# Performance work log

Hardware: AMD Instinct MI355X
Metric: run time of the kernel (lower is better)

Reference implementation:

```python
import jax, jax.numpy as jnp
import numpy as np

B, N = 2, 256
IN_N = 32          # input node features
H = 8              # per-layer default num_heads (GAT does not override it)
HN, HE = 64, 64    # hidden node / edge features per head
DN, DE = HN * H, HE * H  # 512, 512
OUT_N = 32


def _gat_layer(nodes, edges, mask, Wn, bn, We, be, Wa):
    # nodes: [b,n,dn_in], edges: [b,n,n,de_in], mask: [b,n] bool
    nf = nodes @ Wn + bn                                   # [b,n,DN]
    ef = jnp.einsum('bije,ef->bijf', edges, We) + be       # [b,n,n,DE]
    q = nf @ Wa                                            # [b,n,H]
    qe = jnp.einsum('bijf,fh->bijh', ef, Wa)               # [b,n,n,H]
    sn = jnp.einsum('bik,bjk->bij', q, q) / np.float32(np.sqrt(HN))
    se = jnp.einsum('bik,bijk->bij', q, qe) / np.float32(np.sqrt(HE))
    m = mask[..., None]
    wn = jax.nn.softmax(sn * m, axis=-1)                   # [b,n,n]
    we = jax.nn.softmax(se * m, axis=-1)                   # [b,n,n]
    awn = jnp.einsum('bij,bik->bjk', wn, nf)               # [b,n,DN]
    agg_e = jnp.einsum('bij,bijk->bik', we, ef)            # [b,n,DE]
    upd_nodes = nf + awn + agg_e                           # [b,n,DN]
    upd_edges = ef + we[..., None] * ef + jnp.einsum('bij,bik->bijk', wn, nf)
    re = jax.nn.elu(upd_edges)                             # [b,n,n,DE]
    re = (re + jnp.swapaxes(re, 1, 2)) / 2
    return jax.nn.elu(upd_nodes), re


def setup_inputs() -> dict:
    key = jax.random.key(0)
    ks = jax.random.split(key, 16)
    s = 0.05
    return {
        'nodes': jax.random.normal(ks[0], (B, N, IN_N), jnp.float32),
        'edges': jax.random.normal(ks[1], (B, N, N), jnp.float32),
        'node_mask': jnp.ones((B, N), dtype=bool),
        # layer 1 params
        'Wn1': jax.random.normal(ks[2], (IN_N, DN), jnp.float32) * s,
        'bn1': jnp.zeros((DN,), jnp.float32),
        'We1': jax.random.normal(ks[3], (1, DE), jnp.float32) * s,
        'be1': jnp.zeros((DE,), jnp.float32),
        'Wa1': jax.random.normal(ks[4], (DN, H), jnp.float32) * s,
        # layer 2 params
        'Wn2': jax.random.normal(ks[5], (DN, DN), jnp.float32) * s,
        'bn2': jnp.zeros((DN,), jnp.float32),
        'We2': jax.random.normal(ks[6], (DE, DE), jnp.float32) * s,
        'be2': jnp.zeros((DE,), jnp.float32),
        'Wa2': jax.random.normal(ks[7], (DN, H), jnp.float32) * s,
        # final projections
        'Wfn': jax.random.normal(ks[8], (DN, OUT_N), jnp.float32) * s,
        'bfn': jnp.zeros((OUT_N,), jnp.float32),
        'Wfe': jax.random.normal(ks[9], (DE, 1), jnp.float32) * s,
        'bfe': jnp.zeros((1,), jnp.float32),
    }


def reference(nodes, edges, node_mask, Wn1, bn1, We1, be1, Wa1,
              Wn2, bn2, We2, be2, Wa2, Wfn, bfn, Wfe, bfe):
    e = edges[..., None]                      # [b,n,n,1]
    e = (e + jnp.swapaxes(e, 1, 2)) / 2       # symmetrize
    e = jax.nn.relu(e)
    n, e = _gat_layer(nodes, e, node_mask, Wn1, bn1, We1, be1, Wa1)
    n, e = _gat_layer(n, e, node_mask, Wn2, bn2, We2, be2, Wa2)
    out_nodes = jnp.tanh(n @ Wfn + bfn)                                   # [b,n,OUT_N]
    out_edges = jnp.tanh(jnp.einsum('bijf,fo->bijo', e, Wfe) + bfe)[..., 0]  # [b,n,n]
    return out_nodes, out_edges
```

## Files before the change

kernel.cpp:

```cpp
#include <hip/hip_runtime.h>
#include <hip/hip_bf16.h>
#include <stdint.h>


typedef __attribute__((ext_vector_type(8))) short short8v;
typedef __attribute__((ext_vector_type(4))) float f32x4;

#define AS1 __attribute__((address_space(1)))
#define AS3 __attribute__((address_space(3)))

__device__ __forceinline__ float eluf(float x) { return x > 0.f ? x : (__expf(x) - 1.f); }

__device__ __forceinline__ short f2bf(float x) {
  union { float f; unsigned u; } v; v.f = x;
  unsigned r = v.u + 0x7fffu + ((v.u >> 16) & 1u);
  return (short)(r >> 16);
}

template<int OP>
__device__ float blockRed256(float v, float* s4) {
#pragma unroll
  for (int o = 32; o; o >>= 1) { float t = __shfl_xor(v, o); v = OP ? fmaxf(v, t) : v + t; }
  int w = threadIdx.x >> 6;
  __syncthreads();
  if ((threadIdx.x & 63) == 0) s4[w] = v;
  __syncthreads();
  return OP ? fmaxf(fmaxf(s4[0], s4[1]), fmaxf(s4[2], s4[3]))
            : (s4[0] + s4[1] + s4[2] + s4[3]);
}

__global__ void k0a_pack(const float* __restrict__ We2, short* __restrict__ Bp) {
  int id = blockIdx.x * 256 + threadIdx.x;
  int c = id >> 11; int rem = id & 2047; int g = rem >> 9; int n = rem & 511;
  short8v v;
#pragma unroll
  for (int e = 0; e < 8; e++) v[e] = f2bf(We2[(c * 32 + g * 8 + e) * 512 + n]);
  int pos = n * 4 + (g ^ ((n >> 1) & 3));
  *(short8v*)(Bp + (c * 2048 + pos) * 8) = v;
}

__global__ void k0b_prep(const float* __restrict__ We2, const float* __restrict__ Wa2,
                         const float* __restrict__ We1, const float* __restrict__ be1,
                         const float* __restrict__ be2, const float* __restrict__ Wa1,
                         float* __restrict__ M2, float* __restrict__ u1,
                         float* __restrict__ v1, float* __restrict__ vb2) {
  int bx = blockIdx.x; int lane = threadIdx.x;
  if (bx < 512) {
    float a[8] = {0, 0, 0, 0, 0, 0, 0, 0};
    for (int k0 = lane; k0 < 512; k0 += 64) {
      float wv = We2[bx * 512 + k0];
      const float* wa = Wa2 + k0 * 8;
#pragma unroll
      for (int h = 0; h < 8; h++) a[h] += wv * wa[h];
    }
#pragma unroll
    for (int h = 0; h < 8; h++) {
      float v = a[h];
      for (int o = 32; o; o >>= 1) v += __shfl_xor(v, o);
      if (lane == 0) M2[bx * 8 + h] = v;
    }
  } else {
    const float* src = (bx == 512) ? We1 : (bx == 513 ? be1 : be2);
    const float* Wa = (bx == 514) ? Wa2 : Wa1;
    float* dst = (bx == 512) ? u1 : (bx == 513 ? v1 : vb2);
    float a[8] = {0, 0, 0, 0, 0, 0, 0, 0};
    for (int f = lane; f < 512; f += 64) {
      float s = src[f];
#pragma unroll
      for (int h = 0; h < 8; h++) a[h] += s * Wa[f * 8 + h];
    }
#pragma unroll
    for (int h = 0; h < 8; h++) {
      float v = a[h];
      for (int o = 32; o; o >>= 1) v += __shfl_xor(v, o);
      if (lane == 0) dst[h] = v;
    }
  }
}

__global__ __launch_bounds__(512) void k1_nf1(const float* __restrict__ nodes,
    const float* __restrict__ Wn1, const float* __restrict__ bn1,
    const float* __restrict__ Wa1, float* __restrict__ nf1, float* __restrict__ q1) {
  __shared__ float nrow[32];
  __shared__ float qL[8];
  int bi = blockIdx.x; int f = threadIdx.x;
  if (f < 32) nrow[f] = nodes[bi * 32 + f];
  if (f < 8) qL[f] = 0.f;
  __syncthreads();
  float acc = bn1[f];
#pragma unroll 8
  for (int c = 0; c < 32; c++) acc += nrow[c] * Wn1[c * 512 + f];
  nf1[bi * 512 + f] = acc;
  const float* wa = Wa1 + f * 8;
#pragma unroll
  for (int h = 0; h < 8; h++) {
    float v = acc * wa[h];
    for (int o = 32; o; o >>= 1) v += __shfl_xor(v, o);
    if ((f & 63) == 0) atomicAdd(&qL[h], v);
  }
  __syncthreads();
  if (f < 8) q1[bi * 8 + f] = qL[f];
}

__global__ __launch_bounds__(256) void k2_l1attn(const float* __restrict__ edges,
    const float* __restrict__ q1, const float* __restrict__ u1, const float* __restrict__ v1,
    float* __restrict__ e0, float* __restrict__ wn1, float* __restrict__ we1,
    float* __restrict__ tt) {
  __shared__ float s4[4];
  int bi = blockIdx.x; int b = bi >> 8; int i = bi & 255; int j = threadIdx.x;
  float qi[8], qj[8];
#pragma unroll
  for (int h = 0; h < 8; h++) { qi[h] = q1[bi * 8 + h]; qj[h] = q1[(b * 256 + j) * 8 + h]; }
  float eij = edges[bi * 256 + j];
  float eji = edges[(b * 256 + j) * 256 + i];
  float e0v = fmaxf(0.f, 0.5f * (eij + eji));
  e0[bi * 256 + j] = e0v;
  float sn = 0.f, aI = 0.f, cI = 0.f;
#pragma unroll
  for (int h = 0; h < 8; h++) { sn += qi[h] * qj[h]; aI += qi[h] * u1[h]; cI += qi[h] * v1[h]; }
  sn *= 0.125f;
  float se = (aI * e0v + cI) * 0.125f;
  float mn = blockRed256<1>(sn, s4);
  float en = __expf(sn - mn);
  float sumn = blockRed256<0>(en, s4);
  float wnv = en / sumn; wn1[bi * 256 + j] = wnv;
  float me = blockRed256<1>(se, s4);
  float ee = __expf(se - me);
  float sume = blockRed256<0>(ee, s4);
  float wev = ee / sume; we1[bi * 256 + j] = wev;
  float t = blockRed256<0>(wev * e0v, s4);
  if (j == 0) tt[bi] = t;
}

__global__ __launch_bounds__(512) void k3_n1(const float* __restrict__ nf1,
    const float* __restrict__ wn1, const float* __restrict__ tt,
    const float* __restrict__ We1, const float* __restrict__ be1, float* __restrict__ n1) {
  int bx = blockIdx.x; int b = bx >> 8; int x = bx & 255; int k = threadIdx.x;
  float acc = 0.f;
#pragma unroll 4
  for (int i = 0; i < 256; i++) {
    float w = wn1[(b * 256 + i) * 256 + x];
    acc += w * nf1[(b * 256 + i) * 512 + k];
  }
  float t = tt[bx];
  float v = nf1[bx * 512 + k] + acc + t * We1[k] + be1[k];
  n1[bx * 512 + k] = eluf(v);
}

__global__ __launch_bounds__(512) void k4_nf2(const float* __restrict__ n1,
    const float* __restrict__ Wn2, const float* __restrict__ bn2,
    const float* __restrict__ Wa2, const float* __restrict__ M2, const float* __restrict__ vb2,
    float* __restrict__ nf2, float* __restrict__ q2, float* __restrict__ p2,
    float* __restrict__ cst) {
  __shared__ float rowL[512];
  __shared__ float qL[8];
  int bi = blockIdx.x; int k = threadIdx.x;
  rowL[k] = n1[bi * 512 + k];
  if (k < 8) qL[k] = 0.f;
  __syncthreads();
  float acc = bn2[k];
#pragma unroll 4
  for (int g = 0; g < 512; g++) acc += rowL[g] * Wn2[g * 512 + k];
  nf2[bi * 512 + k] = acc;
  const float* wa = Wa2 + k * 8;
#pragma unroll
  for (int h = 0; h < 8; h++) {
    float v = acc * wa[h];
    for (int o = 32; o; o >>= 1) v += __shfl_xor(v, o);
    if ((k & 63) == 0) atomicAdd(&qL[h], v);
  }
  __syncthreads();
  float q[8];
#pragma unroll
  for (int h = 0; h < 8; h++) q[h] = qL[h];
  if (k < 8) q2[bi * 8 + k] = q[k];
  float pv = 0.f; const float* m2 = M2 + k * 8;
#pragma unroll
  for (int h = 0; h < 8; h++) pv += m2[h] * q[h];
  p2[bi * 512 + k] = pv;
  if (k == 0) {
    float c = 0.f;
#pragma unroll
    for (int h = 0; h < 8; h++) c += q[h] * vb2[h];
    cst[bi] = c;
  }
}

__global__ __launch_bounds__(256) void k5a_wn2(const float* __restrict__ q2,
                                               float* __restrict__ wn2) {
  __shared__ float s4[4];
  int bi = blockIdx.x; int b = bi >> 8; int j = threadIdx.x;
  float sn = 0.f;
#pragma unroll
  for (int h = 0; h < 8; h++) sn += q2[bi * 8 + h] * q2[(b * 256 + j) * 8 + h];
  sn *= 0.125f;
  float mn = blockRed256<1>(sn, s4);
  float en = __expf(sn - mn);
  float s = blockRed256<0>(en, s4);
  wn2[bi * 256 + j] = en / s;
}

__global__ __launch_bounds__(256) void k5b_we2(const float* __restrict__ nf1,
    const float* __restrict__ p2, const float* __restrict__ e0,
    const float* __restrict__ wn1, const float* __restrict__ we1,
    const float* __restrict__ We1, const float* __restrict__ be1,
    const float* __restrict__ cst, float* __restrict__ we2) {
  __shared__ float nfiL[512], p2L[512], We1L[512], be1L[512], seL[256], s4[4];
  int bi = blockIdx.x; int b = bi >> 8; int i = bi & 255;
  int tid = threadIdx.x, lane = tid & 63, w = tid >> 6;
  for (int t = tid; t < 512; t += 256) {
    nfiL[t] = nf1[bi * 512 + t]; p2L[t] = p2[bi * 512 + t];
    We1L[t] = We1[t]; be1L[t] = be1[t];
  }
  __syncthreads();
  float cstv = cst[bi];
  int f0 = lane * 8;
  for (int jj = 0; jj < 64; jj++) {
    int j = w * 64 + jj;
    int ij = bi * 256 + j, ji = (b * 256 + j) * 256 + i;
    float e0v = e0[ij];
    float s1 = 1.f + we1[ij]; float w1 = wn1[ij];
    float s2 = 1.f + we1[ji]; float w2 = wn1[ji];
    const float* nj = nf1 + (b * 256 + j) * 512 + f0;
    float4 b0 = *(const float4*)nj;
    float4 b1 = *(const float4*)(nj + 4);
    float njv[8] = {b0.x, b0.y, b0.z, b0.w, b1.x, b1.y, b1.z, b1.w};
    float dot = 0.f;
#pragma unroll
    for (int e = 0; e < 8; e++) {
      float ef = e0v * We1L[f0 + e] + be1L[f0 + e];
      float x1 = ef * s1 + w1 * nfiL[f0 + e];
      float x2 = ef * s2 + w2 * njv[e];
      float e1v = 0.5f * (eluf(x1) + eluf(x2));
      dot += e1v * p2L[f0 + e];
    }
#pragma unroll
    for (int o = 32; o; o >>= 1) dot += __shfl_xor(dot, o);
    if (lane == 0) seL[j] = (dot + cstv) * 0.125f;
  }
  __syncthreads();
  float se = seL[tid];
  float m = blockRed256<1>(se, s4);
  float ee = __expf(se - m);
  float s = blockRed256<0>(ee, s4);
  we2[bi * 256 + tid] = ee / s;
}

__global__ __launch_bounds__(512, 2) void k6_main(
    const float* __restrict__ nf1, const float* __restrict__ nf2,
    const float* __restrict__ e0, const float* __restrict__ wn1, const float* __restrict__ we1,
    const float* __restrict__ wn2, const float* __restrict__ we2,
    const float* __restrict__ We1, const float* __restrict__ be1, const float* __restrict__ be2,
    const float* __restrict__ Wfe, const short* __restrict__ Bp,
    float* __restrict__ aggp, float* __restrict__ Dout) {
  __shared__ __align__(16) short As[4096];
  __shared__ __align__(16) short Bs[16384];
  __shared__ float nf1iL[512], We1L[512], be1L[512], nf2L[512], be2L[512], WfeL[512];
  __shared__ float e0r[128], s1r[128], wnir[128], s2r[128], wnjr[128], weR[128], wnR[128];
  float* aggL = (float*)As;
  float* dsumL = aggL + 512;

  int bid = blockIdx.x; int jb = bid & 1; int bi = bid >> 1; int b = bi >> 8; int i = bi & 255;
  int tid = threadIdx.x, lane = tid & 63, w = tid >> 6;
  int wm = w >> 2, wn_ = w & 3;
  int jbase = jb * 128;

  {
    int t = tid;
    nf1iL[t] = nf1[bi * 512 + t]; We1L[t] = We1[t]; be1L[t] = be1[t];
    nf2L[t] = nf2[bi * 512 + t]; be2L[t] = be2[t]; WfeL[t] = Wfe[t];
  }
  if (tid < 128) {
    int j = jbase + tid; int ij = bi * 256 + j; int ji = (b * 256 + j) * 256 + i;
    e0r[tid] = e0[ij]; s1r[tid] = 1.f + we1[ij]; wnir[tid] = wn1[ij];
    s2r[tid] = 1.f + we1[ji]; wnjr[tid] = wn1[ji];
    weR[tid] = we2[ij]; wnR[tid] = wn2[ij];
  }
  __syncthreads();

  f32x4 acc[4][8];
#pragma unroll
  for (int mi = 0; mi < 4; mi++)
#pragma unroll
    for (int nf = 0; nf < 8; nf++) acc[mi][nf] = (f32x4){0.f, 0.f, 0.f, 0.f};

  int ar = tid >> 2;
  int ac = tid & 3;
  const float* njbase = nf1 + (size_t)(b * 256 + jbase + ar) * 512;
  float e0v = e0r[ar], s1 = s1r[ar], w1 = wnir[ar], s2 = s2r[ar], w2 = wnjr[ar];
  int apos = ar * 4 + (ac ^ ((ar >> 1) & 3));

  for (int cg = 0; cg < 16; cg++) {
    if (cg) __syncthreads();
    {
      const char* g = (const char*)(Bp + cg * 16384);
      char* l = (char*)Bs;
#pragma unroll
      for (int it = 0; it < 4; ++it) {
        int off = it * 8192 + w * 1024;
        __builtin_amdgcn_global_load_lds(
            (const AS1 void*)(g + off + lane * 16),
            (AS3 void*)(l + off), 16, 0, 0);
      }
    }
    {
      int f0 = cg * 32 + ac * 8;
      const float* nj = njbase + f0;
      float4 g0 = *(const float4*)nj;
      float4 g1 = *(const float4*)(nj + 4);
      float njv[8] = {g0.x, g0.y, g0.z, g0.w, g1.x, g1.y, g1.z, g1.w};
      float Wv[8], bv[8], niv[8];
      *(float4*)&Wv[0] = *(const float4*)&We1L[f0]; *(float4*)&Wv[4] = *(const float4*)&We1L[f0 + 4];
      *(float4*)&bv[0] = *(const float4*)&be1L[f0]; *(float4*)&bv[4] = *(const float4*)&be1L[f0 + 4];
      *(float4*)&niv[0] = *(const float4*)&nf1iL[f0]; *(float4*)&niv[4] = *(const float4*)&nf1iL[f0 + 4];
      short8v pk;
#pragma unroll
      for (int e = 0; e < 8; e++) {
        float ef = e0v * Wv[e] + bv[e];
        float x1 = ef * s1 + w1 * niv[e];
        float x2 = ef * s2 + w2 * njv[e];
        float v = 0.5f * (eluf(x1) + eluf(x2));
        pk[e] = f2bf(v);
      }
      *(short8v*)(As + apos * 8) = pk;
    }
    __syncthreads();

    short8v a[4];
    int g_ = lane >> 4;
#pragma unroll
    for (int mi = 0; mi < 4; mi++) {
      int row = wm * 64 + mi * 16 + (lane & 15);
      int cpos = row * 4 + (g_ ^ ((row >> 1) & 3));
      a[mi] = *(const short8v*)(As + cpos * 8);
    }
#pragma unroll
    for (int nf = 0; nf < 8; nf++) {
      int n = wn_ * 128 + nf * 16 + (lane & 15);
      int pos = n * 4 + (g_ ^ ((n >> 1) & 3));
      short8v bf = *(const short8v*)(Bs + pos * 8);
#pragma unroll
      for (int mi = 0; mi < 4; mi++)
        acc[mi][nf] = __builtin_amdgcn_mfma_f32_16x16x32_bf16(a[mi], bf, acc[mi][nf], 0, 0, 0);
    }
  }

  __syncthreads();
  aggL[tid] = 0.f;
  if (tid < 128) dsumL[tid] = 0.f;
  __syncthreads();

  float be2v[8], wfev[8], nf2v[8];
#pragma unroll
  for (int nf = 0; nf < 8; nf++) {
    int k = wn_ * 128 + nf * 16 + (lane & 15);
    be2v[nf] = be2L[k]; wfev[nf] = WfeL[k]; nf2v[nf] = nf2L[k];
  }
  float aggv[8] = {0, 0, 0, 0, 0, 0, 0, 0};
#pragma unroll
  for (int mi = 0; mi < 4; mi++) {
#pragma unroll
    for (int r = 0; r < 4; r++) {
      int jl = wm * 64 + mi * 16 + (lane >> 4) * 4 + r;
      float wE = weR[jl], wN = wnR[jl]; float sE = 1.f + wE;
      float dv = 0.f;
#pragma unroll
      for (int nf = 0; nf < 8; nf++) {
        float ef2 = acc[mi][nf][r] + be2v[nf];
        aggv[nf] += wE * ef2;
        float U = ef2 * sE + wN * nf2v[nf];
        dv += eluf(U) * wfev[nf];
      }
#pragma unroll
      for (int o = 1; o < 16; o <<= 1) dv += __shfl_xor(dv, o);
      if ((lane & 15) == 0) atomicAdd(&dsumL[jl], dv);
    }
  }
#pragma unroll
  for (int nf = 0; nf < 8; nf++) {
    float v = aggv[nf];
    v += __shfl_xor(v, 16); v += __shfl_xor(v, 32);
    if (lane < 16) atomicAdd(&aggL[wn_ * 128 + nf * 16 + lane], v);
  }
  __syncthreads();
  aggp[(bi * 2 + jb) * 512 + tid] = aggL[tid];
  if (tid < 128) Dout[bi * 256 + jbase + tid] = dsumL[tid];
}

__global__ __launch_bounds__(512) void k7_n2(const float* __restrict__ nf2,
    const float* __restrict__ wn2, const float* __restrict__ aggp, float* __restrict__ n2) {
  int bx = blockIdx.x; int b = bx >> 8; int x = bx & 255; int k = threadIdx.x;
  float acc = 0.f;
#pragma unroll 4
  for (int i = 0; i < 256; i++) {
    float w = wn2[(b * 256 + i) * 256 + x];
    acc += w * nf2[(b * 256 + i) * 512 + k];
  }
  float agg = aggp[(bx * 2 + 0) * 512 + k] + aggp[(bx * 2 + 1) * 512 + k];
  n2[bx * 512 + k] = eluf(nf2[bx * 512 + k] + acc + agg);
}

__global__ __launch_bounds__(256) void k8_outn(const float* __restrict__ n2,
    const float* __restrict__ Wfn, const float* __restrict__ bfn, float* __restrict__ outn) {
  __shared__ float rowL[512];
  __shared__ float red[256];
  int bi = blockIdx.x; int tid = threadIdx.x;
  rowL[tid] = n2[bi * 512 + tid];
  rowL[tid + 256] = n2[bi * 512 + tid + 256];
  __syncthreads();
  int o = tid & 31, part = tid >> 5;
  float acc = 0.f;
  for (int f = part * 64; f < part * 64 + 64; f++) acc += rowL[f] * Wfn[f * 32 + o];
  red[tid] = acc;
  __syncthreads();
  if (tid < 32) {
    float s = 0.f;
#pragma unroll
    for (int p = 0; p < 8; p++) s += red[p * 32 + tid];
    outn[bi * 32 + tid] = tanhf(s + bfn[tid]);
  }
}

__global__ __launch_bounds__(256) void k9_oute(const float* __restrict__ D,
    const float* __restrict__ bfe, float* __restrict__ oute) {
  int bi = blockIdx.x; int b = bi >> 8; int i = bi & 255; int j = threadIdx.x;
  float v = 0.5f * (D[bi * 256 + j] + D[(b * 256 + j) * 256 + i]) + bfe[0];
  oute[bi * 256 + j] = tanhf(v);
}

extern "C" void kernel_launch(void* const* d_in, const int* in_sizes, int n_in,
                              void* d_out, int out_size, void* d_ws, size_t ws_size,
                              hipStream_t stream) {
  const float* nodes = (const float*)d_in[0];
  const float* edges = (const float*)d_in[1];
  const float* Wn1 = (const float*)d_in[3];
  const float* bn1 = (const float*)d_in[4];
  const float* We1 = (const float*)d_in[5];
  const float* be1 = (const float*)d_in[6];
  const float* Wa1 = (const float*)d_in[7];
  const float* Wn2 = (const float*)d_in[8];
  const float* bn2 = (const float*)d_in[9];
  const float* We2 = (const float*)d_in[10];
  const float* be2 = (const float*)d_in[11];
  const float* Wa2 = (const float*)d_in[12];
  const float* Wfn = (const float*)d_in[13];
  const float* bfn = (const float*)d_in[14];
  const float* Wfe = (const float*)d_in[15];
  const float* bfe = (const float*)d_in[16];

  float* ws = (float*)d_ws;
  size_t off = 0;
  float* nf1 = ws + off; off += 262144;
  float* q1 = ws + off; off += 4096;
  float* e0 = ws + off; off += 131072;
  float* wn1 = ws + off; off += 131072;
  float* we1 = ws + off; off += 131072;
  float* tt = ws + off; off += 512;
  float* n1 = ws + off; off += 262144;
  float* nf2 = ws + off; off += 262144;
  float* q2 = ws + off; off += 4096;
  float* p2 = ws + off; off += 262144;
  float* cst = ws + off; off += 512;
  float* wn2 = ws + off; off += 131072;
  float* we2 = ws + off; off += 131072;
  float* M2 = ws + off; off += 4096;
  float* u1 = ws + off; off += 8;
  float* v1 = ws + off; off += 8;
  float* vb2 = ws + off; off += 16;
  float* aggp = ws + off; off += 524288;
  float* Dm = ws + off; off += 131072;
  float* n2 = ws + off; off += 262144;
  short* Bp = (short*)(ws + off); off += 131072;

  float* outn = (float*)d_out;
  float* oute = outn + 2 * 256 * 32;

  hipLaunchKernelGGL(k0a_pack, dim3(128), dim3(256), 0, stream, We2, Bp);
  hipLaunchKernelGGL(k0b_prep, dim3(515), dim3(64), 0, stream, We2, Wa2, We1, be1, be2, Wa1,
                     M2, u1, v1, vb2);
  hipLaunchKernelGGL(k1_nf1, dim3(512), dim3(512), 0, stream, nodes, Wn1, bn1, Wa1, nf1, q1);
  hipLaunchKernelGGL(k2_l1attn, dim3(512), dim3(256), 0, stream, edges, q1, u1, v1, e0, wn1,
                     we1, tt);
  hipLaunchKernelGGL(k3_n1, dim3(512), dim3(512), 0, stream, nf1, wn1, tt, We1, be1, n1);
  hipLaunchKernelGGL(k4_nf2, dim3(512), dim3(512), 0, stream, n1, Wn2, bn2, Wa2, M2, vb2,
                     nf2, q2, p2, cst);
  hipLaunchKernelGGL(k5a_wn2, dim3(512), dim3(256), 0, stream, q2, wn2);
  hipLaunchKernelGGL(k5b_we2, dim3(512), dim3(256), 0, stream, nf1, p2, e0, wn1, we1, We1,
                     be1, cst, we2);
  hipLaunchKernelGGL(k6_main, dim3(1024), dim3(512), 0, stream, nf1, nf2, e0, wn1, we1, wn2,
                     we2, We1, be1, be2, Wfe, Bp, aggp, Dm);
  hipLaunchKernelGGL(k7_n2, dim3(512), dim3(512), 0, stream, nf2, wn2, aggp, n2);
  hipLaunchKernelGGL(k8_outn, dim3(512), dim3(256), 0, stream, n2, Wfn, bfn, outn);
  hipLaunchKernelGGL(k9_oute, dim3(512), dim3(256), 0, stream, Dm, bfe, oute);
}
```

Baseline: 306.8 us.

## Exploit edge symmetry: compute each (i,j)/(j,i) tile pair once in k5b and k6

The layer-2 edge-score and main edge GEMM kernels now iterate over upper-triangular 16x16 tile pairs. The symmetric layer-1 edge feature is built once and reused for both the (i,j) and (j,i) outputs, which roughly halves the GEMM and elementwise work. Node aggregation now goes through global atomics into a zero-initialised buffer. The k3, k4 and k7 node kernels each process two rows per block so weight loads are shared, and k6 occupancy hints are raised. The costs are atomic contention, a memset, a serial triangular index decode, and register pressure from the dual epilogue.

```diff
diff --git a/kernel.cpp b/kernel.cpp
--- a/kernel.cpp
+++ b/kernel.cpp
@@ -135,16 +135,20 @@
 __global__ __launch_bounds__(512) void k3_n1(const float* __restrict__ nf1,
     const float* __restrict__ wn1, const float* __restrict__ tt,
     const float* __restrict__ We1, const float* __restrict__ be1, float* __restrict__ n1) {
-  int bx = blockIdx.x; int b = bx >> 8; int x = bx & 255; int k = threadIdx.x;
-  float acc = 0.f;
+  int bx = blockIdx.x;
+  int b = bx >> 7; int x0 = (bx & 127) * 2; int k = threadIdx.x;
+  float acc0 = 0.f, acc1 = 0.f;
 #pragma unroll 4
   for (int i = 0; i < 256; i++) {
-    float w = wn1[(b * 256 + i) * 256 + x];
-    acc += w * nf1[(b * 256 + i) * 512 + k];
-  }
-  float t = tt[bx];
-  float v = nf1[bx * 512 + k] + acc + t * We1[k] + be1[k];
-  n1[bx * 512 + k] = eluf(v);
+    float nv = nf1[(b * 256 + i) * 512 + k];
+    acc0 += wn1[(b * 256 + i) * 256 + x0] * nv;
+    acc1 += wn1[(b * 256 + i) * 256 + x0 + 1] * nv;
+  }
+  float w = We1[k], be = be1[k];
+  int g0 = b * 256 + x0;
+  n1[(size_t)g0 * 512 + k] = eluf(nf1[(size_t)g0 * 512 + k] + acc0 + tt[g0] * w + be);
+  n1[(size_t)(g0 + 1) * 512 + k] =
+      eluf(nf1[(size_t)(g0 + 1) * 512 + k] + acc1 + tt[g0 + 1] * w + be);
 }
 
 __global__ __launch_bounds__(512) void k4_nf2(const float* __restrict__ n1,
@@ -152,42 +156,109 @@
     const float* __restrict__ Wa2, const float* __restrict__ M2, const float* __restrict__ vb2,
     float* __restrict__ nf2, float* __restrict__ q2, float* __restrict__ p2,
     float* __restrict__ cst) {
-  __shared__ float rowL[512];
-  __shared__ float qL[8];
-  int bi = blockIdx.x; int k = threadIdx.x;
-  rowL[k] = n1[bi * 512 + k];
-  if (k < 8) qL[k] = 0.f;
-  __syncthreads();
-  float acc = bn2[k];
+  __shared__ float qL[2][8];
+  int bx = blockIdx.x;
+  int r0 = bx * 2, r1 = r0 + 1;
+  int k = threadIdx.x;
+  if (k < 16) qL[k >> 3][k & 7] = 0.f;
+  __syncthreads();
+  const float* a = n1 + (size_t)r0 * 512;
+  const float* c = n1 + (size_t)r1 * 512;
+  float acc0 = bn2[k], acc1 = bn2[k];
 #pragma unroll 4
-  for (int g = 0; g < 512; g++) acc += rowL[g] * Wn2[g * 512 + k];
-  nf2[bi * 512 + k] = acc;
+  for (int g = 0; g < 512; g++) {
+    float w = Wn2[g * 512 + k];
+    acc0 += a[g] * w; acc1 += c[g] * w;
+  }
+  nf2[(size_t)r0 * 512 + k] = acc0;
+  nf2[(size_t)r1 * 512 + k] = acc1;
   const float* wa = Wa2 + k * 8;
 #pragma unroll
   for (int h = 0; h < 8; h++) {
-    float v = acc * wa[h];
-    for (int o = 32; o; o >>= 1) v += __shfl_xor(v, o);
-    if ((k & 63) == 0) atomicAdd(&qL[h], v);
-  }
-  __syncthreads();
-  float q[8];
-#pragma unroll
-  for (int h = 0; h < 8; h++) q[h] = qL[h];
-  if (k < 8) q2[bi * 8 + k] = q[k];
-  float pv = 0.f; const float* m2 = M2 + k * 8;
-#pragma unroll
-  for (int h = 0; h < 8; h++) pv += m2[h] * q[h];
-  p2[bi * 512 + k] = pv;
+    float v0 = acc0 * wa[h], v1 = acc1 * wa[h];
+    for (int o = 32; o; o >>= 1) { v0 += __shfl_xor(v0, o); v1 += __shfl_xor(v1, o); }
+    if ((k & 63) == 0) { atomicAdd(&qL[0][h], v0); atomicAdd(&qL[1][h], v1); }
+  }
+  __syncthreads();
+  float q0[8], q1v[8];
+#pragma unroll
+  for (int h = 0; h < 8; h++) { q0[h] = qL[0][h]; q1v[h] = qL[1][h]; }
+  if (k < 8) { q2[r0 * 8 + k] = q0[k]; q2[r1 * 8 + k] = q1v[k]; }
+  float p0 = 0.f, p1 = 0.f; const float* m2 = M2 + k * 8;
+#pragma unroll
+  for (int h = 0; h < 8; h++) { p0 += m2[h] * q0[h]; p1 += m2[h] * q1v[h]; }
+  p2[(size_t)r0 * 512 + k] = p0;
+  p2[(size_t)r1 * 512 + k] = p1;
   if (k == 0) {
-    float c = 0.f;
-#pragma unroll
-    for (int h = 0; h < 8; h++) c += q[h] * vb2[h];
-    cst[bi] = c;
-  }
-}
-
-__global__ __launch_bounds__(256) void k5a_wn2(const float* __restrict__ q2,
-                                               float* __restrict__ wn2) {
+    float c0 = 0.f, c1 = 0.f;
+#pragma unroll
+    for (int h = 0; h < 8; h++) { c0 += q0[h] * vb2[h]; c1 += q1v[h] * vb2[h]; }
+    cst[r0] = c0; cst[r1] = c1;
+  }
+}
+
+__global__ __launch_bounds__(256) void k5b_pairs(const float* __restrict__ nf1,
+    const float* __restrict__ p2, const float* __restrict__ e0,
+    const float* __restrict__ wn1, const float* __restrict__ we1,
+    const float* __restrict__ We1, const float* __restrict__ be1,
+    const float* __restrict__ cst, float* __restrict__ se2) {
+  __shared__ float NI[16 * 132], NJ[16 * 132], PI[16 * 132], PJ[16 * 132];
+  __shared__ float W1[128], B1[128];
+  int bid = blockIdx.x; int b = bid & 1; int pr = bid >> 1;
+  int I = 0;
+  { int p = pr; while (p >= 16 - I) { p -= 16 - I; I++; } pr = p; }
+  int J = I + pr;
+  int I0 = I * 16, J0 = J * 16;
+  int tid = threadIdx.x; int ii = tid & 15, jj = tid >> 4;
+  int gi = b * 256 + I0 + ii, gj = b * 256 + J0 + jj;
+  int ij = gi * 256 + (J0 + jj), ji = gj * 256 + (I0 + ii);
+  float e0v = e0[ij];
+  float s1 = 1.f + we1[ij], w1 = wn1[ij];
+  float s2 = 1.f + we1[ji], w2 = wn1[ji];
+  float dot1 = 0.f, dot2 = 0.f;
+  for (int fc = 0; fc < 4; fc++) {
+    __syncthreads();
+    int f00 = fc * 128;
+    for (int t = tid; t < 2048; t += 256) {
+      int row = t >> 7, f = t & 127;
+      NI[row * 132 + f] = nf1[(size_t)(b * 256 + I0 + row) * 512 + f00 + f];
+      NJ[row * 132 + f] = nf1[(size_t)(b * 256 + J0 + row) * 512 + f00 + f];
+      PI[row * 132 + f] = p2[(size_t)(b * 256 + I0 + row) * 512 + f00 + f];
+      PJ[row * 132 + f] = p2[(size_t)(b * 256 + J0 + row) * 512 + f00 + f];
+    }
+    if (tid < 128) { W1[tid] = We1[f00 + tid]; B1[tid] = be1[f00 + tid]; }
+    __syncthreads();
+#pragma unroll 8
+    for (int f = 0; f < 128; f += 4) {
+      float4 niv = *(const float4*)&NI[ii * 132 + f];
+      float4 njv = *(const float4*)&NJ[jj * 132 + f];
+      float4 piv = *(const float4*)&PI[ii * 132 + f];
+      float4 pjv = *(const float4*)&PJ[jj * 132 + f];
+      float4 wv = *(const float4*)&W1[f];
+      float4 bv = *(const float4*)&B1[f];
+      float ni_[4] = {niv.x, niv.y, niv.z, niv.w};
+      float nj_[4] = {njv.x, njv.y, njv.z, njv.w};
+      float pi_[4] = {piv.x, piv.y, piv.z, piv.w};
+      float pj_[4] = {pjv.x, pjv.y, pjv.z, pjv.w};
+      float w_[4] = {wv.x, wv.y, wv.z, wv.w};
+      float b_[4] = {bv.x, bv.y, bv.z, bv.w};
+#pragma unroll
+      for (int e = 0; e < 4; e++) {
+        float ef = e0v * w_[e] + b_[e];
+        float x1 = ef * s1 + w1 * ni_[e];
+        float x2 = ef * s2 + w2 * nj_[e];
+        float e1v = 0.5f * (eluf(x1) + eluf(x2));
+        dot1 += e1v * pi_[e];
+        dot2 += e1v * pj_[e];
+      }
+    }
+  }
+  se2[ij] = (dot1 + cst[gi]) * 0.125f;
+  se2[ji] = (dot2 + cst[gj]) * 0.125f;
+}
+
+__global__ __launch_bounds__(256) void k5ac(const float* __restrict__ q2,
+    const float* __restrict__ se2, float* __restrict__ wn2, float* __restrict__ we2) {
   __shared__ float s4[4];
   int bi = blockIdx.x; int b = bi >> 8; int j = threadIdx.x;
   float sn = 0.f;
@@ -198,83 +269,51 @@
   float en = __expf(sn - mn);
   float s = blockRed256<0>(en, s4);
   wn2[bi * 256 + j] = en / s;
-}
-
-__global__ __launch_bounds__(256) void k5b_we2(const float* __restrict__ nf1,
-    const float* __restrict__ p2, const float* __restrict__ e0,
-    const float* __restrict__ wn1, const float* __restrict__ we1,
-    const float* __restrict__ We1, const float* __restrict__ be1,
-    const float* __restrict__ cst, float* __restrict__ we2) {
-  __shared__ float nfiL[512], p2L[512], We1L[512], be1L[512], seL[256], s4[4];
-  int bi = blockIdx.x; int b = bi >> 8; int i = bi & 255;
-  int tid = threadIdx.x, lane = tid & 63, w = tid >> 6;
-  for (int t = tid; t < 512; t += 256) {
-    nfiL[t] = nf1[bi * 512 + t]; p2L[t] = p2[bi * 512 + t];
-    We1L[t] = We1[t]; be1L[t] = be1[t];
-  }
-  __syncthreads();
-  float cstv = cst[bi];
-  int f0 = lane * 8;
-  for (int jj = 0; jj < 64; jj++) {
-    int j = w * 64 + jj;
-    int ij = bi * 256 + j, ji = (b * 256 + j) * 256 + i;
-    float e0v = e0[ij];
-    float s1 = 1.f + we1[ij]; float w1 = wn1[ij];
-    float s2 = 1.f + we1[ji]; float w2 = wn1[ji];
-    const float* nj = nf1 + (b * 256 + j) * 512 + f0;
-    float4 b0 = *(const float4*)nj;
-    float4 b1 = *(const float4*)(nj + 4);
-    float njv[8] = {b0.x, b0.y, b0.z, b0.w, b1.x, b1.y, b1.z, b1.w};
-    float dot = 0.f;
-#pragma unroll
-    for (int e = 0; e < 8; e++) {
-      float ef = e0v * We1L[f0 + e] + be1L[f0 + e];
-      float x1 = ef * s1 + w1 * nfiL[f0 + e];
-      float x2 = ef * s2 + w2 * njv[e];
-      float e1v = 0.5f * (eluf(x1) + eluf(x2));
-      dot += e1v * p2L[f0 + e];
-    }
-#pragma unroll
-    for (int o = 32; o; o >>= 1) dot += __shfl_xor(dot, o);
-    if (lane == 0) seL[j] = (dot + cstv) * 0.125f;
-  }
-  __syncthreads();
-  float se = seL[tid];
-  float m = blockRed256<1>(se, s4);
-  float ee = __expf(se - m);
-  float s = blockRed256<0>(ee, s4);
-  we2[bi * 256 + tid] = ee / s;
-}
-
-__global__ __launch_bounds__(512, 2) void k6_main(
+  float se = se2[bi * 256 + j];
+  float me = blockRed256<1>(se, s4);
+  float ee = __expf(se - me);
+  float s2 = blockRed256<0>(ee, s4);
+  we2[bi * 256 + j] = ee / s2;
+}
+
+__global__ __launch_bounds__(512, 4) void k6_main(
     const float* __restrict__ nf1, const float* __restrict__ nf2,
     const float* __restrict__ e0, const float* __restrict__ wn1, const float* __restrict__ we1,
     const float* __restrict__ wn2, const float* __restrict__ we2,
     const float* __restrict__ We1, const float* __restrict__ be1, const float* __restrict__ be2,
     const float* __restrict__ Wfe, const short* __restrict__ Bp,
-    float* __restrict__ aggp, float* __restrict__ Dout) {
-  __shared__ __align__(16) short As[4096];
-  __shared__ __align__(16) short Bs[16384];
-  __shared__ float nf1iL[512], We1L[512], be1L[512], nf2L[512], be2L[512], WfeL[512];
-  __shared__ float e0r[128], s1r[128], wnir[128], s2r[128], wnjr[128], weR[128], wnR[128];
-  float* aggL = (float*)As;
-  float* dsumL = aggL + 512;
-
-  int bid = blockIdx.x; int jb = bid & 1; int bi = bid >> 1; int b = bi >> 8; int i = bi & 255;
+    float* __restrict__ agg, float* __restrict__ Dout) {
+  __shared__ __align__(16) char region[40960];
+  short* As = (short*)region;
+  short* Bs = (short*)(region + 8192);
+  float* aggI_L = (float*)region;
+  __shared__ float We1L[512], be1L[512];
+  __shared__ float e0r[128], s1r[128], w1r[128], s2r[128], w2r[128];
+  __shared__ float weAr[128], wnAr[128], weBr[128], wnBr[128];
+  __shared__ float dsumA[128], dsumB[128];
+
+  int bid = blockIdx.x;
+  int b = bid & 1; int rest = bid >> 1;
+  int Jh = rest & 1; int pr = rest >> 1;
+  int I = 0;
+  { int p = pr; while (p >= 16 - I) { p -= 16 - I; I++; } pr = p; }
+  int J = I + pr;
+  int I0 = I * 16, J0 = J * 16 + Jh * 8;
+  bool dual = (I != J);
+
   int tid = threadIdx.x, lane = tid & 63, w = tid >> 6;
   int wm = w >> 2, wn_ = w & 3;
-  int jbase = jb * 128;
-
-  {
-    int t = tid;
-    nf1iL[t] = nf1[bi * 512 + t]; We1L[t] = We1[t]; be1L[t] = be1[t];
-    nf2L[t] = nf2[bi * 512 + t]; be2L[t] = be2[t]; WfeL[t] = Wfe[t];
-  }
+  int g4 = lane >> 4;
+
+  We1L[tid] = We1[tid]; be1L[tid] = be1[tid];
   if (tid < 128) {
-    int j = jbase + tid; int ij = bi * 256 + j; int ji = (b * 256 + j) * 256 + i;
-    e0r[tid] = e0[ij]; s1r[tid] = 1.f + we1[ij]; wnir[tid] = wn1[ij];
-    s2r[tid] = 1.f + we1[ji]; wnjr[tid] = wn1[ji];
-    weR[tid] = we2[ij]; wnR[tid] = wn2[ij];
+    int i = I0 + (tid & 15), j = J0 + (tid >> 4);
+    int ij = (b * 256 + i) * 256 + j, ji = (b * 256 + j) * 256 + i;
+    e0r[tid] = e0[ij];
+    s1r[tid] = 1.f + we1[ij]; w1r[tid] = wn1[ij];
+    s2r[tid] = 1.f + we1[ji]; w2r[tid] = wn1[ji];
+    weAr[tid] = we2[ij]; wnAr[tid] = wn2[ij];
+    weBr[tid] = we2[ji]; wnBr[tid] = wn2[ji];
   }
   __syncthreads();
 
@@ -286,8 +325,9 @@
 
   int ar = tid >> 2;
   int ac = tid & 3;
-  const float* njbase = nf1 + (size_t)(b * 256 + jbase + ar) * 512;
-  float e0v = e0r[ar], s1 = s1r[ar], w1 = wnir[ar], s2 = s2r[ar], w2 = wnjr[ar];
+  const float* nib = nf1 + (size_t)(b * 256 + I0 + (ar & 15)) * 512;
+  const float* njb = nf1 + (size_t)(b * 256 + J0 + (ar >> 4)) * 512;
+  float e0v = e0r[ar], s1 = s1r[ar], w1 = w1r[ar], s2 = s2r[ar], w2 = w2r[ar];
   int apos = ar * 4 + (ac ^ ((ar >> 1) & 3));
 
   for (int cg = 0; cg < 16; cg++) {
@@ -305,14 +345,17 @@
     }
     {
       int f0 = cg * 32 + ac * 8;
-      const float* nj = njbase + f0;
-      float4 g0 = *(const float4*)nj;
-      float4 g1 = *(const float4*)(nj + 4);
-      float njv[8] = {g0.x, g0.y, g0.z, g0.w, g1.x, g1.y, g1.z, g1.w};
-      float Wv[8], bv[8], niv[8];
-      *(float4*)&Wv[0] = *(const float4*)&We1L[f0]; *(float4*)&Wv[4] = *(const float4*)&We1L[f0 + 4];
-      *(float4*)&bv[0] = *(const float4*)&be1L[f0]; *(float4*)&bv[4] = *(const float4*)&be1L[f0 + 4];
-      *(float4*)&niv[0] = *(const float4*)&nf1iL[f0]; *(float4*)&niv[4] = *(const float4*)&nf1iL[f0 + 4];
+      float4 gi0 = *(const float4*)(nib + f0);
+      float4 gi1 = *(const float4*)(nib + f0 + 4);
+      float4 gj0 = *(const float4*)(njb + f0);
+      float4 gj1 = *(const float4*)(njb + f0 + 4);
+      float niv[8] = {gi0.x, gi0.y, gi0.z, gi0.w, gi1.x, gi1.y, gi1.z, gi1.w};
+      float njv[8] = {gj0.x, gj0.y, gj0.z, gj0.w, gj1.x, gj1.y, gj1.z, gj1.w};
+      float Wv[8], bv[8];
+      *(float4*)&Wv[0] = *(const float4*)&We1L[f0];
+      *(float4*)&Wv[4] = *(const float4*)&We1L[f0 + 4];
+      *(float4*)&bv[0] = *(const float4*)&be1L[f0];
+      *(float4*)&bv[4] = *(const float4*)&be1L[f0 + 4];
       short8v pk;
 #pragma unroll
       for (int e = 0; e < 8; e++) {
@@ -327,17 +370,16 @@
     __syncthreads();
 
     short8v a[4];
-    int g_ = lane >> 4;
 #pragma unroll
     for (int mi = 0; mi < 4; mi++) {
       int row = wm * 64 + mi * 16 + (lane & 15);
-      int cpos = row * 4 + (g_ ^ ((row >> 1) & 3));
+      int cpos = row * 4 + (g4 ^ ((row >> 1) & 3));
       a[mi] = *(const short8v*)(As + cpos * 8);
     }
 #pragma unroll
     for (int nf = 0; nf < 8; nf++) {
       int n = wn_ * 128 + nf * 16 + (lane & 15);
-      int pos = n * 4 + (g_ ^ ((n >> 1) & 3));
+      int pos = n * 4 + (g4 ^ ((n >> 1) & 3));
       short8v bf = *(const short8v*)(Bs + pos * 8);
 #pragma unroll
       for (int mi = 0; mi < 4; mi++)
@@ -346,58 +388,109 @@
   }
 
   __syncthreads();
-  aggL[tid] = 0.f;
-  if (tid < 128) dsumL[tid] = 0.f;
-  __syncthreads();
-
-  float be2v[8], wfev[8], nf2v[8];
+  if (tid < 128) { dsumA[tid] = 0.f; dsumB[tid] = 0.f; }
+  __syncthreads();
+
+  float be2v[8], wfev[8];
 #pragma unroll
   for (int nf = 0; nf < 8; nf++) {
     int k = wn_ * 128 + nf * 16 + (lane & 15);
-    be2v[nf] = be2L[k]; wfev[nf] = WfeL[k]; nf2v[nf] = nf2L[k];
-  }
-  float aggv[8] = {0, 0, 0, 0, 0, 0, 0, 0};
+    be2v[nf] = be2[k]; wfev[nf] = Wfe[k];
+  }
+  float aggI[4][8];
+#pragma unroll
+  for (int r4 = 0; r4 < 4; r4++)
+#pragma unroll
+    for (int nf = 0; nf < 8; nf++) aggI[r4][nf] = 0.f;
+
 #pragma unroll
   for (int mi = 0; mi < 4; mi++) {
-#pragma unroll
-    for (int r = 0; r < 4; r++) {
-      int jl = wm * 64 + mi * 16 + (lane >> 4) * 4 + r;
-      float wE = weR[jl], wN = wnR[jl]; float sE = 1.f + wE;
-      float dv = 0.f;
+    int jRow = J0 + wm * 4 + mi;
+    const float* nf2j = nf2 + (size_t)(b * 256 + jRow) * 512;
+    float aggJv[8] = {0, 0, 0, 0, 0, 0, 0, 0};
+#pragma unroll
+    for (int r4 = 0; r4 < 4; r4++) {
+      int jl = wm * 64 + mi * 16 + g4 * 4 + r4;
+      int iRow = I0 + g4 * 4 + r4;
+      const float* nf2i = nf2 + (size_t)(b * 256 + iRow) * 512;
+      float wEA = weAr[jl], sEA = 1.f + weAr[jl], wNA = wnAr[jl];
+      float wEB = weBr[jl], sEB = 1.f + weBr[jl], wNB = wnBr[jl];
+      float dvA = 0.f, dvB = 0.f;
 #pragma unroll
       for (int nf = 0; nf < 8; nf++) {
-        float ef2 = acc[mi][nf][r] + be2v[nf];
-        aggv[nf] += wE * ef2;
-        float U = ef2 * sE + wN * nf2v[nf];
-        dv += eluf(U) * wfev[nf];
+        int k = wn_ * 128 + nf * 16 + (lane & 15);
+        float ef2 = acc[mi][nf][r4] + be2v[nf];
+        aggI[r4][nf] += wEA * ef2;
+        float UA = ef2 * sEA + wNA * nf2i[k];
+        dvA += eluf(UA) * wfev[nf];
+        if (dual) {
+          aggJv[nf] += wEB * ef2;
+          float UB = ef2 * sEB + wNB * nf2j[k];
+          dvB += eluf(UB) * wfev[nf];
+        }
       }
 #pragma unroll
-      for (int o = 1; o < 16; o <<= 1) dv += __shfl_xor(dv, o);
-      if ((lane & 15) == 0) atomicAdd(&dsumL[jl], dv);
-    }
-  }
-#pragma unroll
-  for (int nf = 0; nf < 8; nf++) {
-    float v = aggv[nf];
-    v += __shfl_xor(v, 16); v += __shfl_xor(v, 32);
-    if (lane < 16) atomicAdd(&aggL[wn_ * 128 + nf * 16 + lane], v);
-  }
-  __syncthreads();
-  aggp[(bi * 2 + jb) * 512 + tid] = aggL[tid];
-  if (tid < 128) Dout[bi * 256 + jbase + tid] = dsumL[tid];
+      for (int o = 1; o < 16; o <<= 1) dvA += __shfl_xor(dvA, o);
+      if ((lane & 15) == 0) atomicAdd(&dsumA[jl], dvA);
+      if (dual) {
+#pragma unroll
+        for (int o = 1; o < 16; o <<= 1) dvB += __shfl_xor(dvB, o);
+        if ((lane & 15) == 0) atomicAdd(&dsumB[jl], dvB);
+      }
+    }
+    if (dual) {
+#pragma unroll
+      for (int nf = 0; nf < 8; nf++) {
+        float v = aggJv[nf];
+        v += __shfl_xor(v, 16); v += __shfl_xor(v, 32);
+        if (lane < 16)
+          atomicAdd(&agg[(size_t)(b * 256 + jRow) * 512 + wn_ * 128 + nf * 16 + lane], v);
+      }
+    }
+  }
+
+  __syncthreads();
+  if (wm == 0) {
+#pragma unroll
+    for (int r4 = 0; r4 < 4; r4++)
+#pragma unroll
+      for (int nf = 0; nf < 8; nf++)
+        aggI_L[(g4 * 4 + r4) * 512 + wn_ * 128 + nf * 16 + (lane & 15)] = aggI[r4][nf];
+  }
+  __syncthreads();
+  if (wm == 1) {
+#pragma unroll
+    for (int r4 = 0; r4 < 4; r4++)
+#pragma unroll
+      for (int nf = 0; nf < 8; nf++)
+        aggI_L[(g4 * 4 + r4) * 512 + wn_ * 128 + nf * 16 + (lane & 15)] += aggI[r4][nf];
+  }
+  __syncthreads();
+  for (int t = tid; t < 8192; t += 512)
+    atomicAdd(&agg[(size_t)(b * 256 + I0 + (t >> 9)) * 512 + (t & 511)], aggI_L[t]);
+  if (tid < 128) {
+    int i = I0 + (tid & 15), j = J0 + (tid >> 4);
+    Dout[(size_t)(b * 256 + i) * 256 + j] = dsumA[tid];
+    if (dual) Dout[(size_t)(b * 256 + j) * 256 + i] = dsumB[tid];
+  }
 }
 
 __global__ __launch_bounds__(512) void k7_n2(const float* __restrict__ nf2,
-    const float* __restrict__ wn2, const float* __restrict__ aggp, float* __restrict__ n2) {
-  int bx = blockIdx.x; int b = bx >> 8; int x = bx & 255; int k = threadIdx.x;
-  float acc = 0.f;
+    const float* __restrict__ wn2, const float* __restrict__ agg, float* __restrict__ n2) {
+  int bx = blockIdx.x;
+  int b = bx >> 7; int x0 = (bx & 127) * 2; int k = threadIdx.x;
+  float acc0 = 0.f, acc1 = 0.f;
 #pragma unroll 4
   for (int i = 0; i < 256; i++) {
-    float w = wn2[(b * 256 + i) * 256 + x];
-    acc += w * nf2[(b * 256 + i) * 512 + k];
-  }
-  float agg = aggp[(bx * 2 + 0) * 512 + k] + aggp[(bx * 2 + 1) * 512 + k];
-  n2[bx * 512 + k] = eluf(nf2[bx * 512 + k] + acc + agg);
+    float nv = nf2[(b * 256 + i) * 512 + k];
+    acc0 += wn2[(b * 256 + i) * 256 + x0] * nv;
+    acc1 += wn2[(b * 256 + i) * 256 + x0 + 1] * nv;
+  }
+  int g0 = b * 256 + x0;
+  n2[(size_t)g0 * 512 + k] =
+      eluf(nf2[(size_t)g0 * 512 + k] + acc0 + agg[(size_t)g0 * 512 + k]);
+  n2[(size_t)(g0 + 1) * 512 + k] =
+      eluf(nf2[(size_t)(g0 + 1) * 512 + k] + acc1 + agg[(size_t)(g0 + 1) * 512 + k]);
 }
 
 __global__ __launch_bounds__(256) void k8_outn(const float* __restrict__ n2,
@@ -467,7 +560,8 @@
   float* u1 = ws + off; off += 8;
   float* v1 = ws + off; off += 8;
   float* vb2 = ws + off; off += 16;
-  float* aggp = ws + off; off += 524288;
+  float* se2 = ws + off; off += 131072;
+  float* agg = ws + off; off += 262144;
   float* Dm = ws + off; off += 131072;
   float* n2 = ws + off; off += 262144;
   short* Bp = (short*)(ws + off); off += 131072;
@@ -475,21 +569,22 @@
   float* outn = (float*)d_out;
   float* oute = outn + 2 * 256 * 32;
 
+  hipMemsetAsync(agg, 0, 262144 * sizeof(float), stream);
   hipLaunchKernelGGL(k0a_pack, dim3(128), dim3(256), 0, stream, We2, Bp);
   hipLaunchKernelGGL(k0b_prep, dim3(515), dim3(64), 0, stream, We2, Wa2, We1, be1, be2, Wa1,
                      M2, u1, v1, vb2);
   hipLaunchKernelGGL(k1_nf1, dim3(512), dim3(512), 0, stream, nodes, Wn1, bn1, Wa1, nf1, q1);
   hipLaunchKernelGGL(k2_l1attn, dim3(512), dim3(256), 0, stream, edges, q1, u1, v1, e0, wn1,
                      we1, tt);
-  hipLaunchKernelGGL(k3_n1, dim3(512), dim3(512), 0, stream, nf1, wn1, tt, We1, be1, n1);
-  hipLaunchKernelGGL(k4_nf2, dim3(512), dim3(512), 0, stream, n1, Wn2, bn2, Wa2, M2, vb2,
+  hipLaunchKernelGGL(k3_n1, dim3(256), dim3(512), 0, stream, nf1, wn1, tt, We1, be1, n1);
+  hipLaunchKernelGGL(k4_nf2, dim3(256), dim3(512), 0, stream, n1, Wn2, bn2, Wa2, M2, vb2,
                      nf2, q2, p2, cst);
-  hipLaunchKernelGGL(k5a_wn2, dim3(512), dim3(256), 0, stream, q2, wn2);
-  hipLaunchKernelGGL(k5b_we2, dim3(512), dim3(256), 0, stream, nf1, p2, e0, wn1, we1, We1,
-                     be1, cst, we2);
-  hipLaunchKernelGGL(k6_main, dim3(1024), dim3(512), 0, stream, nf1, nf2, e0, wn1, we1, wn2,
-                     we2, We1, be1, be2, Wfe, Bp, aggp, Dm);
-  hipLaunchKernelGGL(k7_n2, dim3(512), dim3(512), 0, stream, nf2, wn2, aggp, n2);
+  hipLaunchKernelGGL(k5b_pairs, dim3(272), dim3(256), 0, stream, nf1, p2, e0, wn1, we1, We1,
+                     be1, cst, se2);
+  hipLaunchKernelGGL(k5ac, dim3(512), dim3(256), 0, stream, q2, se2, wn2, we2);
+  hipLaunchKernelGGL(k6_main, dim3(544), dim3(512), 0, stream, nf1, nf2, e0, wn1, we1, wn2,
+                     we2, We1, be1, be2, Wfe, Bp, agg, Dm);
+  hipLaunchKernelGGL(k7_n2, dim3(256), dim3(512), 0, stream, nf2, wn2, agg, n2);
   hipLaunchKernelGGL(k8_outn, dim3(512), dim3(256), 0, stream, n2, Wfn, bfn, outn);
   hipLaunchKernelGGL(k9_oute, dim3(512), dim3(256), 0, stream, Dm, bfe, oute);
 }
```

Measured after the change: 874.8 us. +185.2%, slower.
